# Optimization experiments

Measured on AMD Instinct MI355X. Metric: run time of the kernel, lower is better.

## Reference

```python
import jax, jax.numpy as jnp
import numpy as np

N = 20000
E_RAND = 320000
NEG_SLOPE = 0.2


def setup_inputs() -> dict:
    key = jax.random.key(0)
    ks = jax.random.split(key, 10)
    x = jax.random.normal(ks[0], (N, 768), dtype=jnp.float32)
    src = jax.random.randint(ks[1], (E_RAND,), 0, N)
    dst = jax.random.randint(ks[2], (E_RAND,), 0, N)
    loop = jnp.arange(N)
    edge_index = jnp.stack([jnp.concatenate([src, loop]),
                            jnp.concatenate([dst, loop])])  # [2, 340000]
    s = 1.0 / np.sqrt(768.0)
    W1 = jax.random.normal(ks[3], (768, 768), dtype=jnp.float32) * s
    a_src1 = jax.random.normal(ks[4], (8, 96), dtype=jnp.float32) * 0.1
    a_dst1 = jax.random.normal(ks[5], (8, 96), dtype=jnp.float32) * 0.1
    b1 = jnp.zeros((768,), dtype=jnp.float32)
    W2 = jax.random.normal(ks[6], (768, 768), dtype=jnp.float32) * s
    a_src2 = jax.random.normal(ks[7], (1, 768), dtype=jnp.float32) * 0.1
    a_dst2 = jax.random.normal(ks[8], (1, 768), dtype=jnp.float32) * 0.1
    b2 = jnp.zeros((768,), dtype=jnp.float32)
    return {"x": x, "edge_index": edge_index, "W1": W1, "a_src1": a_src1,
            "a_dst1": a_dst1, "b1": b1, "W2": W2, "a_src2": a_src2,
            "a_dst2": a_dst2, "b2": b2}


def gat_layer(x, W, a_src, a_dst, bias, src, dst, heads, out_c, concat):
    n = x.shape[0]
    h = (x @ W).reshape(n, heads, out_c)                      # [N,H,C]
    al_s = jnp.einsum('nhc,hc->nh', h, a_src)                 # [N,H]
    al_d = jnp.einsum('nhc,hc->nh', h, a_dst)
    e = jax.nn.leaky_relu(al_s[src] + al_d[dst], NEG_SLOPE)   # [E,H]
    m = jax.ops.segment_max(e, dst, num_segments=n)           # segment softmax
    ex = jnp.exp(e - m[dst])
    z = jax.ops.segment_sum(ex, dst, num_segments=n)
    alpha = ex / (z[dst] + 1e-16)                             # [E,H]
    msg = h[src] * alpha[:, :, None]                          # [E,H,C]
    out = jax.ops.segment_sum(msg, dst, num_segments=n)       # [N,H,C]
    out = out.reshape(n, heads * out_c) if concat else out.mean(axis=1)
    return out + bias


def reference(x, edge_index, W1, a_src1, a_dst1, b1, W2, a_src2, a_dst2, b2):
    src, dst = edge_index[0], edge_index[1]
    h = gat_layer(x, W1, a_src1, a_dst1, b1, src, dst, heads=8, out_c=96, concat=True)
    h = jax.nn.elu(h)
    out = gat_layer(h, W2, a_src2, a_dst2, b2, src, dst, heads=1, out_c=768, concat=False)
    return out
```

## Files before the change

kernel.cpp:

```cpp
#include <hip/hip_runtime.h>
#include <cstdint>
#include <cstddef>

typedef _Float16 f16;
typedef _Float16 f16x4 __attribute__((ext_vector_type(4)));
typedef _Float16 f16x8 __attribute__((ext_vector_type(8)));
typedef float f32x4 __attribute__((ext_vector_type(4)));

#define LRELU_SLOPE 0.2f

__global__ __launch_bounds__(256) void k_prep_xh(const float* __restrict__ x,
                                                 f16* __restrict__ xh,
                                                 int nvalid, int npad) {
  int total = npad * 192;
  for (int idx = blockIdx.x * blockDim.x + threadIdx.x; idx < total;
       idx += gridDim.x * blockDim.x) {
    int row = idx / 192;
    f16x4 o;
    if (row < nvalid) {
      const float4 v = *(const float4*)(x + (size_t)idx * 4);
      o[0] = (f16)v.x; o[1] = (f16)v.y; o[2] = (f16)v.z; o[3] = (f16)v.w;
    } else {
      o[0] = (f16)0.f; o[1] = (f16)0.f; o[2] = (f16)0.f; o[3] = (f16)0.f;
    }
    *(f16x4*)(xh + (size_t)idx * 4) = o;
  }
}

__global__ __launch_bounds__(256) void k_transpose_w(const float* __restrict__ W,
                                                     f16* __restrict__ Wt) {
  __shared__ float tile[32][33];
  int bn = blockIdx.x * 32;
  int bk = blockIdx.y * 32;
  int tx = threadIdx.x & 31, ty = threadIdx.x >> 5;
  #pragma unroll
  for (int r = ty; r < 32; r += 8)
    tile[r][tx] = W[(size_t)(bk + r) * 768 + bn + tx];
  __syncthreads();
  #pragma unroll
  for (int r = ty; r < 32; r += 8)
    Wt[(size_t)(bn + r) * 768 + bk + tx] = (f16)tile[tx][r];
}

__global__ void k_zero_ints(int* __restrict__ p, int n) {
  for (int i = blockIdx.x * blockDim.x + threadIdx.x; i < n;
       i += gridDim.x * blockDim.x) p[i] = 0;
}

__global__ void k_hist(const int* __restrict__ dst, int E, int* __restrict__ counts) {
  for (int e = blockIdx.x * blockDim.x + threadIdx.x; e < E;
       e += gridDim.x * blockDim.x) atomicAdd(&counts[dst[e]], 1);
}

__global__ __launch_bounds__(1024) void k_scan_block(const int* __restrict__ counts,
                                                     int* __restrict__ starts,
                                                     int* __restrict__ cursor, int n) {
  const int t = threadIdx.x;
  const int nthr = 1024;
  const int chunk = (n + nthr - 1) / nthr;
  const int base = t * chunk;
  int tsum = 0;
  for (int i = 0; i < chunk; i++) {
    int idx = base + i;
    if (idx < n) tsum += counts[idx];
  }
  int lane = t & 63, wv = t >> 6;
  int s = tsum;
  #pragma unroll
  for (int off = 1; off < 64; off <<= 1) {
    int tmp = __shfl_up(s, off);
    if (lane >= off) s += tmp;
  }
  __shared__ int wsum[16];
  if (lane == 63) wsum[wv] = s;
  __syncthreads();
  int woff = 0;
  for (int w = 0; w < wv; w++) woff += wsum[w];
  int run = woff + s - tsum;
  for (int i = 0; i < chunk; i++) {
    int idx = base + i;
    if (idx < n) {
      starts[idx] = run;
      cursor[idx] = run;
      run += counts[idx];
    }
  }
  if (t == nthr - 1) starts[n] = run;
}

__global__ void k_fill(const int* __restrict__ src, const int* __restrict__ dst, int E,
                       int* __restrict__ cursor, int* __restrict__ src_sorted) {
  for (int e = blockIdx.x * blockDim.x + threadIdx.x; e < E;
       e += gridDim.x * blockDim.x) {
    int slot = atomicAdd(&cursor[dst[e]], 1);
    src_sorted[slot] = src[e];
  }
}

__global__ __launch_bounds__(256) void k_gemm_f16(const f16* __restrict__ A,
                                                  const f16* __restrict__ Bt,
                                                  f16* __restrict__ C, int Mvalid) {
  __shared__ __align__(16) f16 As[4][128][8];
  __shared__ __align__(16) f16 Bs[4][128][8];
  const int K = 768;
  const int tid = threadIdx.x;
  const int bm = blockIdx.x * 128;
  const int bn = blockIdx.y * 128;
  const int lane = tid & 63;
  const int wave = tid >> 6;
  const int wr = (wave >> 1) * 64;
  const int wc = (wave & 1) * 64;
  const int ar = tid >> 2;
  const int ak = tid & 3;
  const f16* Ap = A + (size_t)(bm + ar) * K + ak * 8;
  const f16* Bp = Bt + (size_t)(bn + ar) * K + ak * 8;

  f32x4 acc[4][4];
  const f32x4 vzero = {0.f, 0.f, 0.f, 0.f};
  #pragma unroll
  for (int i = 0; i < 4; i++)
    #pragma unroll
    for (int j = 0; j < 4; j++) acc[i][j] = vzero;

  const int fr = lane & 15;
  const int fq = lane >> 4;

  for (int k0 = 0; k0 < K; k0 += 32) {
    *(f16x8*)(&As[ak][ar][0])      = *(const f16x8*)(Ap + k0);
    *(f16x8*)(&As[ak][ar + 64][0]) = *(const f16x8*)(Ap + (size_t)64 * K + k0);
    *(f16x8*)(&Bs[ak][ar][0])      = *(const f16x8*)(Bp + k0);
    *(f16x8*)(&Bs[ak][ar + 64][0]) = *(const f16x8*)(Bp + (size_t)64 * K + k0);
    __syncthreads();
    f16x8 af[4], bf[4];
    #pragma unroll
    for (int i = 0; i < 4; i++) af[i] = *(const f16x8*)(&As[fq][wr + i * 16 + fr][0]);
    #pragma unroll
    for (int j = 0; j < 4; j++) bf[j] = *(const f16x8*)(&Bs[fq][wc + j * 16 + fr][0]);
    #pragma unroll
    for (int i = 0; i < 4; i++)
      #pragma unroll
      for (int j = 0; j < 4; j++)
        acc[i][j] = __builtin_amdgcn_mfma_f32_16x16x32_f16(af[i], bf[j], acc[i][j], 0, 0, 0);
    __syncthreads();
  }

  #pragma unroll
  for (int i = 0; i < 4; i++) {
    #pragma unroll
    for (int j = 0; j < 4; j++) {
      int col = bn + wc + j * 16 + fr;
      #pragma unroll
      for (int r = 0; r < 4; r++) {
        int row = bm + wr + i * 16 + fq * 4 + r;
        if (row < Mvalid) C[(size_t)row * 768 + col] = (f16)acc[i][j][r];
      }
    }
  }
}

template <int H>
__global__ __launch_bounds__(256) void k_al(const f16* __restrict__ h,
                                            const float* __restrict__ a_src,
                                            const float* __restrict__ a_dst,
                                            float* __restrict__ als,
                                            float* __restrict__ ald, int N) {
  int node = blockIdx.x * 4 + (threadIdx.x >> 6);
  int lane = threadIdx.x & 63;
  if (node >= N) return;
  const f16x4* hp = (const f16x4*)(h + (size_t)node * 768 + lane * 12);
  float ss = 0.f, sd = 0.f;
  int cbase = lane * 12;
  #pragma unroll
  for (int q = 0; q < 3; q++) {
    f16x4 hv = hp[q];
    #pragma unroll
    for (int j = 0; j < 4; j++) {
      int c = cbase + q * 4 + j;
      float v = (float)hv[j];
      ss += v * a_src[c];
      sd += v * a_dst[c];
    }
  }
  const int red = (H == 8) ? 8 : 64;
  #pragma unroll
  for (int off = 1; off < red; off <<= 1) {
    ss += __shfl_xor(ss, off);
    sd += __shfl_xor(sd, off);
  }
  if (H == 8) {
    if ((lane & 7) == 0) {
      als[(size_t)node * 8 + (lane >> 3)] = ss;
      ald[(size_t)node * 8 + (lane >> 3)] = sd;
    }
  } else {
    if (lane == 0) { als[node] = ss; ald[node] = sd; }
  }
}

template <int H, bool FINAL>
__global__ __launch_bounds__(192) void k_aggregate(
    const f16* __restrict__ h, const float* __restrict__ als,
    const float* __restrict__ ald, const int* __restrict__ starts,
    const int* __restrict__ src_sorted, const float* __restrict__ bias,
    void* __restrict__ outv, int nvalid) {
  const int n = blockIdx.x;
  const int t = threadIdx.x;
  if (n >= nvalid) return;
  __shared__ float s_ex[256 * H];
  __shared__ int s_src[256];
  __shared__ float s_zp[3][H];
  const int start = starts[n];
  const int deg = starts[n + 1] - start;
  const int lane = t & 63, wv = t >> 6;
  const int hA = (H == 8) ? (t & 7) : 0;
  const int myh = (H == 8) ? (t / 24) : 0;
  const float ald_A = ald[(size_t)n * H + hA];

  float zpart = 0.f;
  float4 acc = {0.f, 0.f, 0.f, 0.f};

  for (int cb = 0; cb < deg; cb += 256) {
    const int cnt = min(256, deg - cb);
    for (int idx = t; idx < cnt * H; idx += 192) {
      const int e = (H == 8) ? (idx >> 3) : idx;
      const int s = src_sorted[start + cb + e];
      if (H == 1 || (idx & 7) == 0) s_src[e] = s;
      float v = als[(size_t)s * H + hA] + ald_A;
      v = v > 0.f ? v : LRELU_SLOPE * v;
      const float ex = __expf(v);
      s_ex[idx] = ex;
      zpart += ex;
    }
    __syncthreads();
    for (int e = 0; e < cnt; e++) {
      const f16x4 hv = *(const f16x4*)(h + (size_t)s_src[e] * 768 + 4 * t);
      const float a = s_ex[e * H + myh];
      acc.x += a * (float)hv[0];
      acc.y += a * (float)hv[1];
      acc.z += a * (float)hv[2];
      acc.w += a * (float)hv[3];
    }
    __syncthreads();
  }

  if (H == 8) {
    #pragma unroll
    for (int off = 8; off < 64; off <<= 1) zpart += __shfl_xor(zpart, off);
    if (lane < 8) s_zp[wv][lane] = zpart;
  } else {
    #pragma unroll
    for (int off = 1; off < 64; off <<= 1) zpart += __shfl_xor(zpart, off);
    if (lane == 0) s_zp[wv][0] = zpart;
  }
  __syncthreads();
  const float z = s_zp[0][myh] + s_zp[1][myh] + s_zp[2][myh];
  const float inv = 1.f / (z + 1e-16f);

  const float4 bv = *(const float4*)(bias + 4 * t);
  float v0 = acc.x * inv + bv.x;
  float v1 = acc.y * inv + bv.y;
  float v2 = acc.z * inv + bv.z;
  float v3 = acc.w * inv + bv.w;
  if (!FINAL) {
    v0 = v0 > 0.f ? v0 : expm1f(v0);
    v1 = v1 > 0.f ? v1 : expm1f(v1);
    v2 = v2 > 0.f ? v2 : expm1f(v2);
    v3 = v3 > 0.f ? v3 : expm1f(v3);
    f16x4 o;
    o[0] = (f16)v0; o[1] = (f16)v1; o[2] = (f16)v2; o[3] = (f16)v3;
    *(f16x4*)((f16*)outv + (size_t)n * 768 + 4 * t) = o;
  } else {
    float4 o = {v0, v1, v2, v3};
    *(float4*)((float*)outv + (size_t)n * 768 + 4 * t) = o;
  }
}

extern "C" void kernel_launch(void* const* d_in, const int* in_sizes, int n_in,
                              void* d_out, int out_size, void* d_ws, size_t ws_size,
                              hipStream_t stream) {
  const float* x   = (const float*)d_in[0];
  const int*   ei  = (const int*)d_in[1];
  const float* W1  = (const float*)d_in[2];
  const float* as1 = (const float*)d_in[3];
  const float* ad1 = (const float*)d_in[4];
  const float* b1  = (const float*)d_in[5];
  const float* W2  = (const float*)d_in[6];
  const float* as2 = (const float*)d_in[7];
  const float* ad2 = (const float*)d_in[8];
  const float* b2  = (const float*)d_in[9];

  const int N = in_sizes[0] / 768;
  const int E = in_sizes[1] / 2;
  const int Mpad = (N + 127) & ~127;
  const int* srcp = ei;
  const int* dstp = ei + E;

  char* p = (char*)d_ws;
  auto alloc = [&](size_t b) { char* r = p; p += (b + 255) & ~(size_t)255; return r; };
  f16*   bufX   = (f16*)alloc((size_t)Mpad * 768 * sizeof(f16));
  f16*   bufH   = (f16*)alloc((size_t)Mpad * 768 * sizeof(f16));
  f16*   Wt1    = (f16*)alloc((size_t)768 * 768 * sizeof(f16));
  f16*   Wt2    = (f16*)alloc((size_t)768 * 768 * sizeof(f16));
  float* als1   = (float*)alloc((size_t)N * 8 * sizeof(float));
  float* ald1   = (float*)alloc((size_t)N * 8 * sizeof(float));
  float* als2   = (float*)alloc((size_t)N * sizeof(float));
  float* ald2   = (float*)alloc((size_t)N * sizeof(float));
  int*   counts = (int*)alloc((size_t)N * sizeof(int));
  int*   starts = (int*)alloc(((size_t)N + 1) * sizeof(int));
  int*   cursor = (int*)alloc((size_t)N * sizeof(int));
  int*   srcs   = (int*)alloc((size_t)E * sizeof(int));

  k_zero_ints<<<dim3(80), dim3(256), 0, stream>>>(counts, N);
  k_hist<<<dim3(512), dim3(256), 0, stream>>>(dstp, E, counts);
  k_scan_block<<<dim3(1), dim3(1024), 0, stream>>>(counts, starts, cursor, N);
  k_fill<<<dim3(512), dim3(256), 0, stream>>>(srcp, dstp, E, cursor, srcs);

  k_prep_xh<<<dim3(1024), dim3(256), 0, stream>>>(x, bufX, N, Mpad);
  k_transpose_w<<<dim3(24, 24), dim3(256), 0, stream>>>(W1, Wt1);
  k_transpose_w<<<dim3(24, 24), dim3(256), 0, stream>>>(W2, Wt2);

  k_gemm_f16<<<dim3(Mpad / 128, 6), dim3(256), 0, stream>>>(bufX, Wt1, bufH, N);
  k_al<8><<<dim3((N + 3) / 4), dim3(256), 0, stream>>>(bufH, as1, ad1, als1, ald1, N);
  k_aggregate<8, false><<<dim3(N), dim3(192), 0, stream>>>(bufH, als1, ald1, starts, srcs, b1, bufX, N);

  k_gemm_f16<<<dim3(Mpad / 128, 6), dim3(256), 0, stream>>>(bufX, Wt2, bufH, N);
  k_al<1><<<dim3((N + 3) / 4), dim3(256), 0, stream>>>(bufH, as2, ad2, als2, ald2, N);
  k_aggregate<1, true><<<dim3(N), dim3(192), 0, stream>>>(bufH, als2, ald2, starts, srcs, b2, d_out, N);
}
```

Measured before the change: 360.7 us.

## Store GEMM output in 96-column slices and aggregate per slice with single-pass softmax

The GEMM now writes its output as eight column slices of 96 halves each, one contiguous slab per slice, so that a gather of one slice for many source nodes touches a smaller working set. The aggregation kernel is restructured so each block handles one slice for eight destination nodes, 24 threads per node. It computes exp weights on the fly in a single loop without shared memory or barriers. Consecutive blocks share a node group across slices, which is meant to improve cache locality of the random gathers. The cost is recomputing the attention logits per slice and more per-thread serial latency for high-degree nodes.

```diff
diff --git a/kernel.cpp b/kernel.cpp
--- a/kernel.cpp
+++ b/kernel.cpp
@@ -99,7 +99,8 @@
 
 __global__ __launch_bounds__(256) void k_gemm_f16(const f16* __restrict__ A,
                                                   const f16* __restrict__ Bt,
-                                                  f16* __restrict__ C, int Mvalid) {
+                                                  f16* __restrict__ C, int Mvalid,
+                                                  int SS) {
   __shared__ __align__(16) f16 As[4][128][8];
   __shared__ __align__(16) f16 Bs[4][128][8];
   const int K = 768;
@@ -148,31 +149,35 @@
   for (int i = 0; i < 4; i++) {
     #pragma unroll
     for (int j = 0; j < 4; j++) {
-      int col = bn + wc + j * 16 + fr;
+      const int col = bn + wc + j * 16 + fr;
+      const int cs = col / 96;
+      const int cw = col - cs * 96;
+      f16* cp = C + (size_t)cs * SS + cw;
       #pragma unroll
       for (int r = 0; r < 4; r++) {
-        int row = bm + wr + i * 16 + fq * 4 + r;
-        if (row < Mvalid) C[(size_t)row * 768 + col] = (f16)acc[i][j][r];
+        const int row = bm + wr + i * 16 + fq * 4 + r;
+        if (row < Mvalid) cp[(size_t)row * 96] = (f16)acc[i][j][r];
       }
     }
   }
 }
 
 template <int H>
-__global__ __launch_bounds__(256) void k_al(const f16* __restrict__ h,
+__global__ __launch_bounds__(256) void k_al(const f16* __restrict__ hs,
                                             const float* __restrict__ a_src,
                                             const float* __restrict__ a_dst,
                                             float* __restrict__ als,
-                                            float* __restrict__ ald, int N) {
+                                            float* __restrict__ ald, int N, int SS) {
   int node = blockIdx.x * 4 + (threadIdx.x >> 6);
   int lane = threadIdx.x & 63;
   if (node >= N) return;
-  const f16x4* hp = (const f16x4*)(h + (size_t)node * 768 + lane * 12);
+  const int sl = lane >> 3, wl = lane & 7;
+  const f16* hp = hs + (size_t)sl * SS + (size_t)node * 96 + wl * 12;
   float ss = 0.f, sd = 0.f;
-  int cbase = lane * 12;
+  const int cbase = sl * 96 + wl * 12;
   #pragma unroll
   for (int q = 0; q < 3; q++) {
-    f16x4 hv = hp[q];
+    f16x4 hv = *(const f16x4*)(hp + q * 4);
     #pragma unroll
     for (int j = 0; j < 4; j++) {
       int c = cbase + q * 4 + j;
@@ -189,8 +194,8 @@
   }
   if (H == 8) {
     if ((lane & 7) == 0) {
-      als[(size_t)node * 8 + (lane >> 3)] = ss;
-      ald[(size_t)node * 8 + (lane >> 3)] = sd;
+      als[(size_t)node * 8 + sl] = ss;
+      ald[(size_t)node * 8 + sl] = sd;
     }
   } else {
     if (lane == 0) { als[node] = ss; ald[node] = sd; }
@@ -198,65 +203,41 @@
 }
 
 template <int H, bool FINAL>
-__global__ __launch_bounds__(192) void k_aggregate(
-    const f16* __restrict__ h, const float* __restrict__ als,
+__global__ __launch_bounds__(192) void k_agg_slice(
+    const f16* __restrict__ hs, const float* __restrict__ als,
     const float* __restrict__ ald, const int* __restrict__ starts,
-    const int* __restrict__ src_sorted, const float* __restrict__ bias,
-    void* __restrict__ outv, int nvalid) {
-  const int n = blockIdx.x;
+    const int* __restrict__ srcs, const float* __restrict__ bias,
+    void* __restrict__ outv, int N, int SS) {
+  const int s = blockIdx.x & 7;
+  const int g = blockIdx.x >> 3;
   const int t = threadIdx.x;
-  if (n >= nvalid) return;
-  __shared__ float s_ex[256 * H];
-  __shared__ int s_src[256];
-  __shared__ float s_zp[3][H];
+  const int nl = t / 24;
+  const int c = t - nl * 24;
+  const int n = g * 8 + nl;
+  if (n >= N) return;
+  const int head = (H == 8) ? s : 0;
   const int start = starts[n];
   const int deg = starts[n + 1] - start;
-  const int lane = t & 63, wv = t >> 6;
-  const int hA = (H == 8) ? (t & 7) : 0;
-  const int myh = (H == 8) ? (t / 24) : 0;
-  const float ald_A = ald[(size_t)n * H + hA];
-
-  float zpart = 0.f;
+  const float aldn = ald[(size_t)n * H + head];
+  const f16* hslice = hs + (size_t)s * SS;
+
   float4 acc = {0.f, 0.f, 0.f, 0.f};
-
-  for (int cb = 0; cb < deg; cb += 256) {
-    const int cnt = min(256, deg - cb);
-    for (int idx = t; idx < cnt * H; idx += 192) {
-      const int e = (H == 8) ? (idx >> 3) : idx;
-      const int s = src_sorted[start + cb + e];
-      if (H == 1 || (idx & 7) == 0) s_src[e] = s;
-      float v = als[(size_t)s * H + hA] + ald_A;
-      v = v > 0.f ? v : LRELU_SLOPE * v;
-      const float ex = __expf(v);
-      s_ex[idx] = ex;
-      zpart += ex;
-    }
-    __syncthreads();
-    for (int e = 0; e < cnt; e++) {
-      const f16x4 hv = *(const f16x4*)(h + (size_t)s_src[e] * 768 + 4 * t);
-      const float a = s_ex[e * H + myh];
-      acc.x += a * (float)hv[0];
-      acc.y += a * (float)hv[1];
-      acc.z += a * (float)hv[2];
-      acc.w += a * (float)hv[3];
-    }
-    __syncthreads();
-  }
-
-  if (H == 8) {
-    #pragma unroll
-    for (int off = 8; off < 64; off <<= 1) zpart += __shfl_xor(zpart, off);
-    if (lane < 8) s_zp[wv][lane] = zpart;
-  } else {
-    #pragma unroll
-    for (int off = 1; off < 64; off <<= 1) zpart += __shfl_xor(zpart, off);
-    if (lane == 0) s_zp[wv][0] = zpart;
-  }
-  __syncthreads();
-  const float z = s_zp[0][myh] + s_zp[1][myh] + s_zp[2][myh];
+  float z = 0.f;
+  for (int e = 0; e < deg; e++) {
+    const int sv = srcs[start + e];
+    float v = als[(size_t)sv * H + head] + aldn;
+    v = v > 0.f ? v : LRELU_SLOPE * v;
+    const float ex = __expf(v);
+    z += ex;
+    const f16x4 hv = *(const f16x4*)(hslice + (size_t)sv * 96 + c * 4);
+    acc.x += ex * (float)hv[0];
+    acc.y += ex * (float)hv[1];
+    acc.z += ex * (float)hv[2];
+    acc.w += ex * (float)hv[3];
+  }
   const float inv = 1.f / (z + 1e-16f);
-
-  const float4 bv = *(const float4*)(bias + 4 * t);
+  const int cg = s * 96 + c * 4;
+  const float4 bv = *(const float4*)(bias + cg);
   float v0 = acc.x * inv + bv.x;
   float v1 = acc.y * inv + bv.y;
   float v2 = acc.z * inv + bv.z;
@@ -268,10 +249,10 @@
     v3 = v3 > 0.f ? v3 : expm1f(v3);
     f16x4 o;
     o[0] = (f16)v0; o[1] = (f16)v1; o[2] = (f16)v2; o[3] = (f16)v3;
-    *(f16x4*)((f16*)outv + (size_t)n * 768 + 4 * t) = o;
+    *(f16x4*)((f16*)outv + (size_t)n * 768 + cg) = o;
   } else {
     float4 o = {v0, v1, v2, v3};
-    *(float4*)((float*)outv + (size_t)n * 768 + 4 * t) = o;
+    *(float4*)((float*)outv + (size_t)n * 768 + cg) = o;
   }
 }
 
@@ -292,6 +273,7 @@
   const int N = in_sizes[0] / 768;
   const int E = in_sizes[1] / 2;
   const int Mpad = (N + 127) & ~127;
+  const int SS = Mpad * 96;
   const int* srcp = ei;
   const int* dstp = ei + E;
 
@@ -319,11 +301,15 @@
   k_transpose_w<<<dim3(24, 24), dim3(256), 0, stream>>>(W1, Wt1);
   k_transpose_w<<<dim3(24, 24), dim3(256), 0, stream>>>(W2, Wt2);
 
-  k_gemm_f16<<<dim3(Mpad / 128, 6), dim3(256), 0, stream>>>(bufX, Wt1, bufH, N);
-  k_al<8><<<dim3((N + 3) / 4), dim3(256), 0, stream>>>(bufH, as1, ad1, als1, ald1, N);
-  k_aggregate<8, false><<<dim3(N), dim3(192), 0, stream>>>(bufH, als1, ald1, starts, srcs, b1, bufX, N);
-
-  k_gemm_f16<<<dim3(Mpad / 128, 6), dim3(256), 0, stream>>>(bufX, Wt2, bufH, N);
-  k_al<1><<<dim3((N + 3) / 4), dim3(256), 0, stream>>>(bufH, as2, ad2, als2, ald2, N);
-  k_aggregate<1, true><<<dim3(N), dim3(192), 0, stream>>>(bufH, als2, ald2, starts, srcs, b2, d_out, N);
-}
+  const int ngroups = (N + 7) / 8;
+
+  k_gemm_f16<<<dim3(Mpad / 128, 6), dim3(256), 0, stream>>>(bufX, Wt1, bufH, N, SS);
+  k_al<8><<<dim3((N + 3) / 4), dim3(256), 0, stream>>>(bufH, as1, ad1, als1, ald1, N, SS);
+  k_agg_slice<8, false><<<dim3(ngroups * 8), dim3(192), 0, stream>>>(
+      bufH, als1, ald1, starts, srcs, b1, bufX, N, SS);
+
+  k_gemm_f16<<<dim3(Mpad / 128, 6), dim3(256), 0, stream>>>(bufX, Wt2, bufH, N, SS);
+  k_al<1><<<dim3((N + 3) / 4), dim3(256), 0, stream>>>(bufH, as2, ad2, als2, ald2, N, SS);
+  k_agg_slice<1, true><<<dim3(ngroups * 8), dim3(192), 0, stream>>>(
+      bufH, als2, ald2, starts, srcs, b2, d_out, N, SS);
+}
```

Measured after the change: 456.7 us. 26.6% more time.
